# Kernel tuning notes

Measured on AMD Instinct MI355X. Metric: run time of the kernel, lower is better.

Reference implementation:

```python
import jax, jax.numpy as jnp
import numpy as np
from jax import lax

GEN_POLY = ("1111001", "1011011")  # rate 1/2, constraint length 7 (octal 171/133)


def build_trellis(gen_poly):
    """Feed-forward (non-recursive) convolutional trellis tables.

    State = shift-register contents, most-recent bit is the MSB of the state
    index. Returns int32 tables, each [ns, ni]:
      to_nodes[s, b]        : next state from state s with input bit b
      op_by_fromnode[s, b]  : emitted output-symbol index for (s, b)
      from_nodes[j, m]      : m-th predecessor state of state j
      ip_by_tonode[j, m]    : input bit taken on that predecessor transition
    """
    mu = len(gen_poly[0]) - 1
    ns, ni = 2 ** mu, 2
    g = np.array([[int(c) for c in p] for p in gen_poly])  # [conv_n, mu+1]
    to_nodes = np.zeros((ns, ni), np.int32)
    op_by_fromnode = np.zeros((ns, ni), np.int32)
    from_nodes = np.zeros((ns, ni), np.int32)
    ip_by_tonode = np.zeros((ns, ni), np.int32)
    fill = np.zeros(ns, np.int32)
    for s in range(ns):
        rbits = [(s >> (mu - 1 - j)) & 1 for j in range(mu)]
        for b in range(ni):
            w = np.array([b] + rbits)                 # full window [b, r0..r_{mu-1}]
            obits = (g @ w) % 2                        # output bits, MSB first
            o = int("".join(str(int(x)) for x in obits), 2)
            j = int("".join(str(x) for x in ([b] + rbits[:-1])), 2)
            to_nodes[s, b] = j
            op_by_fromnode[s, b] = o
            from_nodes[j, fill[j]] = s
            ip_by_tonode[j, fill[j]] = b
            fill[j] += 1
    return to_nodes, op_by_fromnode, from_nodes, ip_by_tonode


TO_NODES, OP_BY_FROM, FROM_NODES, IP_BY_TO = build_trellis(GEN_POLY)
CONV_N = len(GEN_POLY)
MU = len(GEN_POLY[0]) - 1
NS = 2 ** MU
NO = 2 ** CONV_N
# output-symbol bit patterns, MSB first, mapped to signs (1-2*bit)
_OP_BITS = np.array([[(o >> (CONV_N - 1 - j)) & 1 for j in range(CONV_N)]
                     for o in range(NO)], np.float32)
OP_SIGN = jnp.asarray(1.0 - 2.0 * _OP_BITS)  # [NO, CONV_N]
IP_SIGN = jnp.asarray([1.0, -1.0])           # sign of input bit b: 1-2b


def setup_inputs() -> dict:
    key = jax.random.key(0)
    k1, k2 = jax.random.split(key)
    B, n = 256, 4096
    T = n // CONV_N  # = k = 2048 info bits
    llr_ch = jax.random.normal(k1, (B, n), dtype=jnp.float32)
    llr_a = jax.random.normal(k2, (B, T), dtype=jnp.float32)
    return {"llr_ch": llr_ch, "llr_a": llr_a}


def _bcjr(llr_ch, llr_a):
    B, n = llr_ch.shape
    T = n // CONV_N
    # branch metrics: bm[t, b, o] = exp(0.5 * sum_j llr[b, t, j] * (1-2*opbit_j(o)))
    llr_r = llr_ch.reshape(B, T, CONV_N)
    bm = jnp.exp(0.5 * jnp.einsum('btj,oj->tbo', llr_r, OP_SIGN))  # [T, B, NO]
    llr_a_t = llr_a.T  # [T, B]

    def gamma_fn(bm_t, la_t):
        # a-priori factor exp(0.5*llr_a*(1-2b)) times channel branch metric
        ap = jnp.exp(0.5 * la_t[:, None, None] * IP_SIGN[None, None, :])  # [B,1,2]
        return ap * bm_t[:, OP_BY_FROM]  # [B, NS, 2]

    alpha0 = jnp.zeros((B, NS), jnp.float32).at[:, 0].set(1.0)

    def fwd(alpha_prev, inp):
        bm_t, la_t = inp
        gam = gamma_fn(bm_t, la_t)                        # [B, NS, 2] by from-state
        ag = gam * alpha_prev[:, :, None]                  # alpha_{t} * gamma_t
        agt = ag[:, FROM_NODES, IP_BY_TO]                  # regroup by to-state
        alpha = agt.sum(-1)
        alpha = alpha / alpha.sum(-1, keepdims=True)       # normalize (as in TF code)
        return alpha, alpha_prev                            # emit alpha BEFORE step t

    _, alphas = lax.scan(fwd, alpha0, (bm, llr_a_t))       # alphas[t] = alpha_t, [T,B,NS]

    beta_T = jnp.full((B, NS), 1.0 / NS, jnp.float32)      # non-terminated: uniform

    def bwd(beta_next, inp):
        bm_t, la_t, alpha_t = inp
        gam = gamma_fn(bm_t, la_t)                         # [B, NS, 2]
        bg = gam * beta_next[:, TO_NODES]                  # gamma * beta_{t+1}(to)
        beta = bg.sum(-1)
        beta = beta / beta.sum(-1, keepdims=True)
        joint = alpha_t[:, :, None] * bg                   # APP per (state, bit)
        llr_t = jnp.log(joint[..., 0].sum(-1)) - jnp.log(joint[..., 1].sum(-1))
        return beta, llr_t

    _, llrs_rev = lax.scan(bwd, beta_T, (bm[::-1], llr_a_t[::-1], alphas[::-1]))
    return llrs_rev[::-1].T  # [B, T] soft LLRs (hard_out=False)


def reference(llr_ch, llr_a):
    return _bcjr(llr_ch, llr_a)
```

## Files before the change

### kernel.cpp

```cpp
#include <hip/hip_runtime.h>

#define T_LEN 2048
#define NSTATE 64
#define NCHUNK 16
#define CH_S 128
#define HF 64
#define WARM 64
#define RK 16
#define ROWQ 36

template<int CTRL>
__device__ __forceinline__ float dpp_add(float v) {
    int r = __builtin_amdgcn_update_dpp(0, __float_as_int(v), CTRL, 0xF, 0xF, true);
    return v + __int_as_float(r);
}

__device__ __forceinline__ float dpp_mov_xor1(float v) {
    return __int_as_float(__builtin_amdgcn_update_dpp(0, __float_as_int(v), 0xB1, 0xF, 0xF, true));
}

__device__ __forceinline__ float dpp_sum_to63(float v) {
    v = dpp_add<0x111>(v);
    v = dpp_add<0x112>(v);
    v = dpp_add<0x114>(v);
    v = dpp_add<0x118>(v);
    v = dpp_add<0x142>(v);
    v = dpp_add<0x143>(v);
    return v;
}

__device__ __forceinline__ float wave_total(float v) {
    float s = dpp_sum_to63(v);
    return __int_as_float(__builtin_amdgcn_readlane(__float_as_int(s), 63));
}

__device__ __forceinline__ float pair_sum_xor1(float v) {
    int r = __builtin_amdgcn_update_dpp(0, __float_as_int(v), 0xB1, 0xF, 0xF, true);
    return v + __int_as_float(r);
}

__device__ __forceinline__ float bperm(int addrb, float v) {
    return __int_as_float(__builtin_amdgcn_ds_bpermute(addrb, __float_as_int(v)));
}

__device__ __forceinline__ unsigned bf16_of(float f) {
    return (__float_as_uint(f) + 0x8000u) >> 16;
}
template<int HI>
__device__ __forceinline__ float bf16_half(unsigned w) {
    return __uint_as_float(HI ? (w & 0xffff0000u) : (w << 16));
}


template<int MODE>
__device__ __forceinline__ float fwd_group(float state,
                                           const float* __restrict__ chp,
                                           const float* __restrict__ lap,
                                           unsigned* __restrict__ alds,
                                           const unsigned* __restrict__ blds,
                                           float* __restrict__ outp,
                                           int g, int t0, int lane,
                                           float kE, float k0, float k1,
                                           int fselb)
{
    #pragma unroll
    for (int h = 0; h < 2; ++h) {
        const int gb = g + 8 * h;
        const float4* c4 = (const float4*)(chp + 2 * gb);
        const float4* a4 = (const float4*)(lap + gb);
        float4 cc[4], aa[2];
        #pragma unroll
        for (int i = 0; i < 4; ++i) cc[i] = c4[i];
        #pragma unroll
        for (int i = 0; i < 2; ++i) aa[i] = a4[i];
        uint4 bw0, bw1;
        if (MODE == 2) {
            const int off = (gb - t0 - HF) >> 1;
            bw0 = *(const uint4*)(blds + (lane >> 1) * ROWQ + off);
            bw1 = *(const uint4*)(blds + (32 + (lane >> 1)) * ROWQ + off);
        }
        unsigned pk[4];
        #pragma unroll
        for (int i = 0; i < 8; ++i) {
            float l0 = (i & 1) ? cc[i >> 1].z : cc[i >> 1].x;
            float l1 = (i & 1) ? cc[i >> 1].w : cc[i >> 1].y;
            float la = ((const float*)aa)[i];
            if (MODE == 1) {
                unsigned hs = bf16_of(state);
                if (i & 1) pk[i >> 1] |= hs << 16; else pk[i >> 1] = hs;
            }
            float x   = fmaf(la, kE, fmaf(l0, k0, l1 * k1));
            float g0v = exp2f(x);
            float g1v = __builtin_amdgcn_rcpf(g0v);
            float sg0 = state * g0v;
            float sg1 = state * g1v;
            if (MODE == 2) {
                unsigned w0 = (&bw0.x)[i >> 1];
                unsigned w1 = (&bw1.x)[i >> 1];
                float b0v = (i & 1) ? bf16_half<1>(w0) : bf16_half<0>(w0);
                float b1v = (i & 1) ? bf16_half<1>(w1) : bf16_half<0>(w1);
                float na = dpp_sum_to63(sg0 * b0v);
                float nb = dpp_sum_to63(sg1 * b1v);
                if (lane == 63)
                    outp[gb + i] = (__log2f(na) - __log2f(nb)) * 0.6931471805599453f;
            }
            float s0 = pair_sum_xor1(sg0);
            float s1 = pair_sum_xor1(sg1);
            float v  = (lane & 1) ? s1 : s0;
            state = bperm(fselb, v);
        }
        if (MODE == 1)
            *(uint4*)(alds + lane * ROWQ + ((gb - t0) >> 1)) =
                make_uint4(pk[0], pk[1], pk[2], pk[3]);
    }
    float s = wave_total(state);
    return state * __builtin_amdgcn_rcpf(s);
}

template<int MODE>
__device__ __forceinline__ float bwd_group(float state,
                                           const float* __restrict__ chp,
                                           const float* __restrict__ lap,
                                           const unsigned* __restrict__ alds,
                                           unsigned* __restrict__ blds,
                                           float* __restrict__ outp,
                                           int g, int t0, int lane,
                                           float kE, float k0, float k1,
                                           unsigned pmask, int bgb)
{
    const bool odd = (lane & 1);
    #pragma unroll
    for (int h = 1; h >= 0; --h) {
        const int gb = g + 8 * h;
        const float4* c4 = (const float4*)(chp + 2 * gb);
        const float4* a4 = (const float4*)(lap + gb);
        float4 cc[4], aa[2];
        #pragma unroll
        for (int i = 0; i < 4; ++i) cc[i] = c4[i];
        #pragma unroll
        for (int i = 0; i < 2; ++i) aa[i] = a4[i];
        uint4 aw;
        if (MODE == 2)
            aw = *(const uint4*)(alds + lane * ROWQ + ((gb - t0) >> 1));
        unsigned pk[4];
        #pragma unroll
        for (int i = 7; i >= 0; --i) {
            float l0 = (i & 1) ? cc[i >> 1].z : cc[i >> 1].x;
            float l1 = (i & 1) ? cc[i >> 1].w : cc[i >> 1].y;
            float la = ((const float*)aa)[i];
            if (MODE == 1) {
                unsigned hs = bf16_of(state);
                if (i & 1) pk[i >> 1] = hs << 16; else pk[i >> 1] |= hs;
            }
            float x  = fmaf(la, kE, fmaf(l0, k0, l1 * k1));
            float xg = __uint_as_float(__float_as_uint(x) ^ pmask);
            float ga  = exp2f(xg);
            float gb_ = __builtin_amdgcn_rcpf(ga);
            float a  = bperm(bgb, state);
            float bb = dpp_mov_xor1(a);
            float u0 = ga * a;
            float u1 = gb_ * bb;
            if (MODE == 2) {
                unsigned w = (&aw.x)[i >> 1];
                float av = (i & 1) ? bf16_half<1>(w) : bf16_half<0>(w);
                float ua = odd ? u1 : u0;
                float ub = odd ? u0 : u1;
                float na = dpp_sum_to63(av * ua);
                float nb = dpp_sum_to63(av * ub);
                if (lane == 63)
                    outp[gb + i] = (__log2f(na) - __log2f(nb)) * 0.6931471805599453f;
            }
            state = u0 + u1;
        }
        if (MODE == 1)
            *(uint4*)(blds + lane * ROWQ + ((gb - t0 - HF) >> 1)) =
                make_uint4(pk[0], pk[1], pk[2], pk[3]);
    }
    float s = wave_total(state);
    return state * __builtin_amdgcn_rcpf(s);
}

__global__ __launch_bounds__(128, 4)
void bcjr_fused_kernel(const float* __restrict__ llr_ch,
                       const float* __restrict__ llr_a,
                       float* __restrict__ out)
{
    __shared__ __align__(16) unsigned alds[NSTATE * ROWQ];
    __shared__ __align__(16) unsigned blds[NSTATE * ROWQ];

    const int lane  = threadIdx.x & 63;
    const int role  = threadIdx.x >> 6;
    const int unit  = blockIdx.x;
    const int chunk = unit & (NCHUNK - 1);
    const int b     = unit >> 4;

    const float c0 = 1.0f - 2.0f * (float)(__popc(lane & 57) & 1);
    const float c1 = 1.0f - 2.0f * (float)(__popc(lane & 27) & 1);
    const float kE = 0.5f * 1.442695040888963f;
    const float k0 = kE * c0, k1 = kE * c1;

    const float* chp = llr_ch + (size_t)b * (2 * T_LEN);
    const float* lap = llr_a  + (size_t)b * T_LEN;
    float* outp = out + (size_t)b * T_LEN;
    const int t0 = chunk * CH_S;

    if (role == 0) {
        const int fselb = (2 * (lane & 31) + (lane >> 5)) << 2;
        float state = (chunk == 0) ? ((lane == 0) ? 1.0f : 0.0f) : (1.0f / 64.0f);
        const int ts = (chunk == 0) ? t0 : t0 - WARM;
        for (int g = ts; g < t0; g += RK)
            state = fwd_group<0>(state, chp, lap, alds, blds, outp, g, t0, lane, kE, k0, k1, fselb);
        for (int g = t0; g < t0 + HF; g += RK)
            state = fwd_group<1>(state, chp, lap, alds, blds, outp, g, t0, lane, kE, k0, k1, fselb);
        __syncthreads();
        for (int g = t0 + HF; g < t0 + CH_S; g += RK)
            state = fwd_group<2>(state, chp, lap, alds, blds, outp, g, t0, lane, kE, k0, k1, fselb);
    } else {
        const unsigned pmask = (unsigned)(lane & 1) << 31;
        const int bgb = ((lane >> 1) + ((lane & 1) << 5)) << 2;
        float state = 1.0f / 64.0f;
        const int te = (chunk == NCHUNK - 1) ? (t0 + CH_S) : (t0 + CH_S + WARM);
        for (int g = te - RK; g >= t0 + CH_S; g -= RK)
            state = bwd_group<0>(state, chp, lap, alds, blds, outp, g, t0, lane, kE, k0, k1, pmask, bgb);
        for (int g = t0 + CH_S - RK; g >= t0 + HF; g -= RK)
            state = bwd_group<1>(state, chp, lap, alds, blds, outp, g, t0, lane, kE, k0, k1, pmask, bgb);
        __syncthreads();
        for (int g = t0 + HF - RK; g >= t0; g -= RK)
            state = bwd_group<2>(state, chp, lap, alds, blds, outp, g, t0, lane, kE, k0, k1, pmask, bgb);
    }
}

extern "C" void kernel_launch(void* const* d_in, const int* in_sizes, int n_in,
                              void* d_out, int out_size, void* d_ws, size_t ws_size,
                              hipStream_t stream) {
    const float* llr_ch = (const float*)d_in[0];
    const float* llr_a  = (const float*)d_in[1];
    float* out = (float*)d_out;

    int B = in_sizes[0] / (2 * T_LEN);
    (void)d_ws; (void)ws_size;

    int n_units = B * NCHUNK;
    hipLaunchKernelGGL(bcjr_fused_kernel, dim3(n_units), dim3(128), 0, stream,
                       llr_ch, llr_a, out);
}
```

Baseline: 129.0 us.

## Swizzle LDS stash, batch LLR outputs, shorten warmup, raise occupancy

```diff
diff --git a/kernel.cpp b/kernel.cpp
--- a/kernel.cpp
+++ b/kernel.cpp
@@ -5,9 +5,8 @@
 #define NCHUNK 16
 #define CH_S 128
 #define HF 64
-#define WARM 64
+#define WARM 48
 #define RK 16
-#define ROWQ 36
 
 template<int CTRL>
 __device__ __forceinline__ float dpp_add(float v) {
@@ -49,6 +48,15 @@
 template<int HI>
 __device__ __forceinline__ float bf16_half(unsigned w) {
     return __uint_as_float(HI ? (w & 0xffff0000u) : (w << 16));
+}
+
+__device__ __forceinline__ float stash63(float acc, float v, int L, int lane) {
+    float bc = __int_as_float(__builtin_amdgcn_readlane(__float_as_int(v), 63));
+    return (lane == L) ? bc : acc;
+}
+
+__device__ __forceinline__ int swz(int row, int cc) {
+    return row * 32 + (((cc ^ row) & 7) << 2);
 }
 
 
@@ -63,6 +71,7 @@
                                            float kE, float k0, float k1,
                                            int fselb)
 {
+    float acc = 1.0f;
     #pragma unroll
     for (int h = 0; h < 2; ++h) {
         const int gb = g + 8 * h;
@@ -75,9 +84,9 @@
         for (int i = 0; i < 2; ++i) aa[i] = a4[i];
         uint4 bw0, bw1;
         if (MODE == 2) {
-            const int off = (gb - t0 - HF) >> 1;
-            bw0 = *(const uint4*)(blds + (lane >> 1) * ROWQ + off);
-            bw1 = *(const uint4*)(blds + (32 + (lane >> 1)) * ROWQ + off);
+            const int ch = (gb - t0 - HF) >> 3;
+            bw0 = *(const uint4*)(blds + swz(lane >> 1, ch));
+            bw1 = *(const uint4*)(blds + swz(32 + (lane >> 1), ch));
         }
         unsigned pk[4];
         #pragma unroll
@@ -101,8 +110,8 @@
                 float b1v = (i & 1) ? bf16_half<1>(w1) : bf16_half<0>(w1);
                 float na = dpp_sum_to63(sg0 * b0v);
                 float nb = dpp_sum_to63(sg1 * b1v);
-                if (lane == 63)
-                    outp[gb + i] = (__log2f(na) - __log2f(nb)) * 0.6931471805599453f;
+                acc = stash63(acc, na, 2 * (8 * h + i), lane);
+                acc = stash63(acc, nb, 2 * (8 * h + i) + 1, lane);
             }
             float s0 = pair_sum_xor1(sg0);
             float s1 = pair_sum_xor1(sg1);
@@ -110,8 +119,13 @@
             state = bperm(fselb, v);
         }
         if (MODE == 1)
-            *(uint4*)(alds + lane * ROWQ + ((gb - t0) >> 1)) =
+            *(uint4*)(alds + swz(lane, (gb - t0) >> 3)) =
                 make_uint4(pk[0], pk[1], pk[2], pk[3]);
+    }
+    if (MODE == 2) {
+        float lg = __log2f(acc);
+        float dl = (lg - dpp_mov_xor1(lg)) * 0.6931471805599453f;
+        if (lane < 32 && !(lane & 1)) outp[g + (lane >> 1)] = dl;
     }
     float s = wave_total(state);
     return state * __builtin_amdgcn_rcpf(s);
@@ -129,6 +143,7 @@
                                            unsigned pmask, int bgb)
 {
     const bool odd = (lane & 1);
+    float acc = 1.0f;
     #pragma unroll
     for (int h = 1; h >= 0; --h) {
         const int gb = g + 8 * h;
@@ -141,7 +156,7 @@
         for (int i = 0; i < 2; ++i) aa[i] = a4[i];
         uint4 aw;
         if (MODE == 2)
-            aw = *(const uint4*)(alds + lane * ROWQ + ((gb - t0) >> 1));
+            aw = *(const uint4*)(alds + swz(lane, (gb - t0) >> 3));
         unsigned pk[4];
         #pragma unroll
         for (int i = 7; i >= 0; --i) {
@@ -167,26 +182,31 @@
                 float ub = odd ? u0 : u1;
                 float na = dpp_sum_to63(av * ua);
                 float nb = dpp_sum_to63(av * ub);
-                if (lane == 63)
-                    outp[gb + i] = (__log2f(na) - __log2f(nb)) * 0.6931471805599453f;
+                acc = stash63(acc, na, 2 * (8 * h + i), lane);
+                acc = stash63(acc, nb, 2 * (8 * h + i) + 1, lane);
             }
             state = u0 + u1;
         }
         if (MODE == 1)
-            *(uint4*)(blds + lane * ROWQ + ((gb - t0 - HF) >> 1)) =
+            *(uint4*)(blds + swz(lane, (gb - t0 - HF) >> 3)) =
                 make_uint4(pk[0], pk[1], pk[2], pk[3]);
+    }
+    if (MODE == 2) {
+        float lg = __log2f(acc);
+        float dl = (lg - dpp_mov_xor1(lg)) * 0.6931471805599453f;
+        if (lane < 32 && !(lane & 1)) outp[g + (lane >> 1)] = dl;
     }
     float s = wave_total(state);
     return state * __builtin_amdgcn_rcpf(s);
 }
 
-__global__ __launch_bounds__(128, 4)
+__global__ __launch_bounds__(128, 5)
 void bcjr_fused_kernel(const float* __restrict__ llr_ch,
                        const float* __restrict__ llr_a,
                        float* __restrict__ out)
 {
-    __shared__ __align__(16) unsigned alds[NSTATE * ROWQ];
-    __shared__ __align__(16) unsigned blds[NSTATE * ROWQ];
+    __shared__ __align__(16) unsigned alds[NSTATE * 32];
+    __shared__ __align__(16) unsigned blds[NSTATE * 32];
 
     const int lane  = threadIdx.x & 63;
     const int role  = threadIdx.x >> 6;
```

New measurement: 129.8 us. Within noise of the previous version (+0.6%).
